# Optimization experiments

Measured on AMD Instinct MI355X. Metric: run time of the kernel, lower is better.

Reference implementation:

```python
import jax, jax.numpy as jnp
import numpy as np
import math

B, T, IN, H, OUT, L = 8, 256, 128, 128, 128, 2
MAX_EP_LEN = 10000.0


def _rotate(x, pos, d):
    # rope as in source: repeat(1,1,2) = concat along last dim (not interleave)
    half = jnp.exp(jnp.arange(0, d, 2, dtype=jnp.float32) * (-math.log(MAX_EP_LEN) / d))  # [d/2]
    ang = pos[..., None] * half  # [B,T,d/2]
    sine = jnp.concatenate([jnp.sin(ang), jnp.sin(ang)], axis=-1)
    cos = jnp.concatenate([jnp.cos(ang), jnp.cos(ang)], axis=-1)
    y1, y2 = jnp.split(x, 2, axis=-1)
    x_rot = jnp.concatenate([-y2, y1], axis=-1)
    return x * cos + x_rot * sine


def _layernorm(x, w, b, eps=1e-5):
    m = jnp.mean(x, axis=-1, keepdims=True)
    v = jnp.mean((x - m) ** 2, axis=-1, keepdims=True)
    return (x - m) / jnp.sqrt(v + eps) * w + b


def _block(x, S0, Z0, Wk, Wq, Wv, lw, lb, w1, b1, w2, b2, scw, scb):
    # x: [B,T,F]; S0: [B,F,F]; Z0: [B,F]
    x = _layernorm(x, lw, lb)
    K = jax.nn.elu(x @ Wk.T) + 1.0
    Q = jax.nn.elu(x @ Wq.T) + 1.0
    V = x @ Wv.T
    outer = jnp.einsum('bti,btj->btij', K, V)  # [B,T,F,F]
    S = jnp.clip(jnp.cumsum(outer, axis=1), -1e20, 1e20) + S0[:, None]  # [B,T,F,F]
    Z = jnp.clip(jnp.cumsum(K, axis=1), -1e20, 1e20) + Z0[:, None]      # [B,T,F]
    num = jnp.einsum('bti,btil->btl', Q, S)
    den = jnp.einsum('bti,bti->bt', Q, Z)[..., None] + 1e-5
    out = num / den
    out = jax.nn.relu(jax.nn.relu(out @ w1.T + b1) @ w2.T + b2)  # feed_forward
    out = out + x @ scw.T + scb                                   # residual shortcut
    return out, S[:, -1], Z[:, -1]


def setup_inputs() -> dict:
    key = jax.random.key(0)
    ks = jax.random.split(key, 14)
    s = 0.05
    return {
        'z': jax.random.normal(ks[0], (T, B, IN), jnp.float32),
        'state': jnp.zeros((B, L * (H * H + H) + 1), jnp.float32),
        'Wk': jax.random.normal(ks[1], (L, H, IN), jnp.float32) * s,
        'Wq': jax.random.normal(ks[2], (L, H, IN), jnp.float32) * s,
        'Wv': jax.random.normal(ks[3], (L, H, IN), jnp.float32) * s,
        'ln_w': jnp.ones((L, IN), jnp.float32),
        'ln_b': jnp.zeros((L, IN), jnp.float32),
        'ff_w1': jax.random.normal(ks[4], (L, H, H), jnp.float32) * s,
        'ff_b1': jnp.zeros((L, H), jnp.float32),
        'ff_w2': jax.random.normal(ks[5], (L, H, H), jnp.float32) * s,
        'ff_b2': jnp.zeros((L, H), jnp.float32),
        'sc_w': jax.random.normal(ks[6], (L, H, IN), jnp.float32) * s,
        'sc_b': jnp.zeros((L, H), jnp.float32),
        'unmap_w': jax.random.normal(ks[7], (OUT, H), jnp.float32) * s,
        'unmap_b': jnp.zeros((OUT,), jnp.float32),
    }


def reference(z, state, Wk, Wq, Wv, ln_w, ln_b, ff_w1, ff_b1, ff_w2, ff_b2, sc_w, sc_b, unmap_w, unmap_b):
    x = jnp.transpose(z, (1, 0, 2))  # [B,T,IN]
    ts = state[:, -1]                # [B] timestep counters
    core = state[:, :-1].reshape(B, L, H * H + H)
    pos = ts[:, None] + jnp.arange(T, dtype=jnp.float32)[None, :]  # [B,T]
    x = _rotate(x, pos, IN)  # embedding_type == 'rope'
    new_states = []
    for i in range(L):
        S0 = core[:, i, :H * H].reshape(B, H, H)
        Z0 = core[:, i, H * H:]
        x, Sl, Zl = _block(x, S0, Z0, Wk[i], Wq[i], Wv[i], ln_w[i], ln_b[i],
                           ff_w1[i], ff_b1[i], ff_w2[i], ff_b2[i], sc_w[i], sc_b[i])
        new_states.append(jnp.concatenate([Sl.reshape(B, -1), Zl], axis=-1))
    y = x @ unmap_w.T + unmap_b
    st = jnp.concatenate([jnp.stack(new_states, axis=1).reshape(B, -1), (ts + T)[:, None]], axis=-1)
    return jnp.transpose(y, (1, 0, 2)), st
```

## Files before the change

kernel.cpp:

```cpp
#include <hip/hip_runtime.h>
#include <math.h>

#define Bn 8
#define Tn 256
#define COREn 16512
#define SDn   33025

typedef __attribute__((ext_vector_type(8))) short short8;
typedef __attribute__((ext_vector_type(4))) short short4v;
typedef __attribute__((ext_vector_type(4))) float floatx4;

#define MFMA16(a,b,c) __builtin_amdgcn_mfma_f32_16x16x32_bf16(a,b,c,0,0,0)

static __device__ __forceinline__ unsigned short f2bf(float f) {
  unsigned int u = __float_as_uint(f);
  return (unsigned short)((u + 0x7FFFu + ((u >> 16) & 1u)) >> 16);
}
static __device__ __forceinline__ float bf2f(unsigned short h) {
  return __uint_as_float((unsigned int)h << 16);
}
static __device__ __forceinline__ short8 ldwfrag(const float* p) {
  float4 a = *(const float4*)p;
  float4 b = *(const float4*)(p + 4);
  short8 r;
  r[0] = (short)f2bf(a.x); r[1] = (short)f2bf(a.y);
  r[2] = (short)f2bf(a.z); r[3] = (short)f2bf(a.w);
  r[4] = (short)f2bf(b.x); r[5] = (short)f2bf(b.y);
  r[6] = (short)f2bf(b.z); r[7] = (short)f2bf(b.w);
  return r;
}
static __device__ __forceinline__ void ld8(const float* p, float* v) {
  float4 a = *(const float4*)p, b = *(const float4*)(p + 4);
  v[0]=a.x; v[1]=a.y; v[2]=a.z; v[3]=a.w; v[4]=b.x; v[5]=b.y; v[6]=b.z; v[7]=b.w;
}

static __device__ __forceinline__ void proj_epilogue(
    int by, int g0, int b, int t0l, int n0, int n1, int quad,
    floatx4 acc0, floatx4 acc1,
    unsigned short* __restrict__ Kb, unsigned short* __restrict__ Kt,
    unsigned short* __restrict__ Qb, unsigned short* __restrict__ Vt,
    unsigned short* __restrict__ skipb, const float* __restrict__ scb) {
  if (by == 0) {
    short4v kt0, kt1;
#pragma unroll
    for (int j = 0; j < 4; j++) {
      int row = quad * 4 + j;
      float e0 = acc0[j] > 0.f ? acc0[j] + 1.f : expf(acc0[j]);
      float e1 = acc1[j] > 0.f ? acc1[j] + 1.f : expf(acc1[j]);
      Kb[(size_t)(g0 + row) * 128 + n0] = f2bf(e0);
      Kb[(size_t)(g0 + row) * 128 + n1] = f2bf(e1);
      kt0[j] = (short)f2bf(e0); kt1[j] = (short)f2bf(e1);
    }
    *(short4v*)(Kt + (size_t)(b * 128 + n0) * 256 + t0l + quad * 4) = kt0;
    *(short4v*)(Kt + (size_t)(b * 128 + n1) * 256 + t0l + quad * 4) = kt1;
  } else if (by == 1) {
#pragma unroll
    for (int j = 0; j < 4; j++) {
      int row = quad * 4 + j;
      float e0 = acc0[j] > 0.f ? acc0[j] + 1.f : expf(acc0[j]);
      float e1 = acc1[j] > 0.f ? acc1[j] + 1.f : expf(acc1[j]);
      Qb[(size_t)(g0 + row) * 128 + n0] = f2bf(e0);
      Qb[(size_t)(g0 + row) * 128 + n1] = f2bf(e1);
    }
  } else if (by == 2) {
    short4v v0, v1;
#pragma unroll
    for (int j = 0; j < 4; j++) { v0[j] = (short)f2bf(acc0[j]); v1[j] = (short)f2bf(acc1[j]); }
    *(short4v*)(Vt + (size_t)(b * 128 + n0) * 256 + t0l + quad * 4) = v0;
    *(short4v*)(Vt + (size_t)(b * 128 + n1) * 256 + t0l + quad * 4) = v1;
  } else {
    float sb0 = scb[n0], sb1 = scb[n1];
#pragma unroll
    for (int j = 0; j < 4; j++) {
      int row = quad * 4 + j;
      skipb[(size_t)(g0 + row) * 128 + n0] = f2bf(acc0[j] + sb0);
      skipb[(size_t)(g0 + row) * 128 + n1] = f2bf(acc1[j] + sb1);
    }
  }
}

__global__ __launch_bounds__(256, 1) void prep_kernel(
    const float* __restrict__ z, const float* __restrict__ state,
    const float* __restrict__ Wk, const float* __restrict__ Wq,
    const float* __restrict__ Wv, const float* __restrict__ scw,
    const float* __restrict__ lnw, const float* __restrict__ lnb,
    const float* __restrict__ scb,
    const float* __restrict__ w1all, const float* __restrict__ w2all,
    const float* __restrict__ unw,
    unsigned short* __restrict__ Kb0, unsigned short* __restrict__ Qb0,
    unsigned short* __restrict__ Kt0, unsigned short* __restrict__ Vt0,
    unsigned short* __restrict__ skip0, unsigned short* __restrict__ S0t,
    float* __restrict__ warm_sink) {
  const int tid = threadIdx.x, bx = blockIdx.x;
  if (bx < 512) {
    __shared__ unsigned short xs[16][136];
    const int lane = tid & 63, wv = tid >> 6, lm = lane & 15, quad = lane >> 4;
    const int tile = bx >> 2, by = bx & 3;
    const int g0 = tile * 16;
    const int r = tid >> 4, c0 = (tid & 15) * 8;
    const int g = g0 + r, b = g >> 8, t = g & 255;
    const int n0 = wv * 32 + lm, n1 = n0 + 16;

    float v[8], pv[8];
    const float* zr = z + ((size_t)t * Bn + b) * 128;
    ld8(zr + c0, v);
    ld8(zr + (c0 ^ 64), pv);
    const float* W = by == 0 ? Wk : by == 1 ? Wq : by == 2 ? Wv : scw;
    short8 bA[4], bB[4];
#pragma unroll
    for (int kc = 0; kc < 4; kc++) {
      bA[kc] = ldwfrag(W + (size_t)n0 * 128 + kc * 32 + quad * 8);
      bB[kc] = ldwfrag(W + (size_t)n1 * 128 + kc * 32 + quad * 8);
    }
    float pos = state[(size_t)b * SDn + SDn - 1] + (float)t;

#pragma unroll
    for (int i = 0; i < 8; i++) {
      int jj = (c0 + i) & 63;
      float ang = pos * expf((float)jj * -0.14391156831212787f);
      float sn = sinf(ang), cs = cosf(ang);
      v[i] = (c0 < 64) ? (v[i] * cs - pv[i] * sn) : (v[i] * cs + pv[i] * sn);
    }
    float sm = 0.f, sq = 0.f;
#pragma unroll
    for (int i = 0; i < 8; i++) { sm += v[i]; sq += v[i] * v[i]; }
    for (int d = 8; d; d >>= 1) { sm += __shfl_xor(sm, d, 16); sq += __shfl_xor(sq, d, 16); }
    float mean = sm * (1.f / 128.f);
    float rstd = rsqrtf(sq * (1.f / 128.f) - mean * mean + 1e-5f);
    short8 xv;
#pragma unroll
    for (int i = 0; i < 8; i++)
      xv[i] = (short)f2bf((v[i] - mean) * rstd * lnw[c0 + i] + lnb[c0 + i]);
    *(short8*)&xs[r][c0] = xv;
    __syncthreads();

    const int bb = g0 >> 8, t0l = g0 & 255;
    floatx4 a0 = {0.f,0.f,0.f,0.f}, a1 = {0.f,0.f,0.f,0.f};
#pragma unroll
    for (int kc = 0; kc < 4; kc++) {
      short8 a = *(const short8*)&xs[lm][kc * 32 + quad * 8];
      a0 = MFMA16(a, bA[kc], a0);
      a1 = MFMA16(a, bB[kc], a1);
    }
    proj_epilogue(by, g0, bb, t0l, n0, n1, quad, a0, a1,
                  Kb0, Kt0, Qb0, Vt0, skip0, scb);
  } else if (bx < 528) {
    __shared__ float tl[32][33];
    const int id = bx - 512, b = id >> 1, l = id & 1;
    const float* src = state + (size_t)b * SDn + (size_t)l * COREn;
    unsigned short* dst = S0t + (size_t)(l * 8 + b) * 16384;
    const int r = tid >> 3, c4 = (tid & 7) * 4;
#pragma unroll
    for (int tI = 0; tI < 4; tI++)
      for (int tJ = 0; tJ < 4; tJ++) {
        int i0 = tI * 32, j0 = tJ * 32;
#pragma unroll
        for (int q = 0; q < 4; q++)
          tl[r][c4 + q] = src[(size_t)(i0 + r) * 128 + j0 + c4 + q];
        __syncthreads();
        short4v o;
#pragma unroll
        for (int q = 0; q < 4; q++) o[q] = (short)f2bf(tl[c4 + q][r]);
        *(short4v*)(dst + (size_t)(j0 + r) * 128 + i0 + c4) = o;
        __syncthreads();
      }
  } else {
    const int wb = bx - 528;
    const float* ptrs[9] = { w1all, w1all + 16384, w2all, w2all + 16384, unw,
                             Wk + 16384, Wq + 16384, Wv + 16384, scw + 16384 };
    float acc = 0.f;
#pragma unroll
    for (int i = 0; i < 9; i++) {
      float4 vv = ((const float4*)ptrs[i])[wb * 256 + tid];
      acc += vv.x + vv.y + vv.z + vv.w;
    }
    if (acc == 1234567.89f) warm_sink[0] = acc;
  }
}

static __device__ void state_upd(
    int tid, int idx, int l,
    const unsigned short* __restrict__ Kt, const unsigned short* __restrict__ Vt,
    const float* __restrict__ state, float* __restrict__ st_out) {
  const int lane = tid & 63, wv = tid >> 6, lm = lane & 15, quad = lane >> 4;
  const int b = idx >> 4, sub = idx & 15;
  const int i0 = (sub >> 1) * 16, j0 = (sub & 1) * 64;
  const size_t sb = (size_t)b * SDn + (size_t)l * COREn;
  short8 ka[8], vb[8];
#pragma unroll
  for (int kc = 0; kc < 8; kc++) {
    ka[kc] = *(const short8*)(Kt + (size_t)(b * 128 + i0 + lm) * 256 + kc * 32 + quad * 8);
    vb[kc] = *(const short8*)(Vt + (size_t)(b * 128 + j0 + wv * 16 + lm) * 256 + kc * 32 + quad * 8);
  }
  floatx4 acc = {0.f, 0.f, 0.f, 0.f};
#pragma unroll
  for (int kc = 0; kc < 8; kc++) acc = MFMA16(ka[kc], vb[kc], acc);
#pragma unroll
  for (int j = 0; j < 4; j++) {
    size_t off = sb + (size_t)(i0 + quad * 4 + j) * 128 + j0 + wv * 16 + lm;
    st_out[off] = acc[j] + state[off];
  }
  if (j0 == 0) {
    if (tid < 128) {
      int i = tid >> 3, seg = tid & 7;
      const unsigned short* kr = Kt + (size_t)(b * 128 + i0 + i) * 256 + seg * 32;
      float zs = 0.f;
#pragma unroll
      for (int x = 0; x < 4; x++) {
        short8 kv = *(const short8*)(kr + x * 8);
#pragma unroll
        for (int y = 0; y < 8; y++) zs += bf2f((unsigned short)kv[y]);
      }
      for (int d = 4; d; d >>= 1) zs += __shfl_xor(zs, d, 8);
      if (seg == 0) {
        size_t zo = sb + 16384 + i0 + i;
        st_out[zo] = zs + state[zo];
      }
    }
    if (sub == 0 && tid == 0 && l == 0)
      st_out[(size_t)b * SDn + SDn - 1] = state[(size_t)b * SDn + SDn - 1] + 256.f;
  }
}

__global__ __launch_bounds__(256, 1) void attn_kernel(
    const unsigned short* __restrict__ Kb, const unsigned short* __restrict__ Qb,
    const unsigned short* __restrict__ Vt, const unsigned short* __restrict__ Kt,
    const unsigned short* __restrict__ S0tl, const float* __restrict__ state,
    unsigned short* __restrict__ attnb, float* __restrict__ st_out, int l) {
  const int tid = threadIdx.x, bx = blockIdx.x;
  const int lane = tid & 63, wv = tid >> 6, lm = lane & 15, quad = lane >> 4;
  if (bx < 256) {
    __shared__ unsigned short xs[16][136];
    __shared__ unsigned short Ssc[4][16][40];
    __shared__ float Obuf[4][16][68];
    __shared__ float Z0s[128];
    __shared__ float denw[4][16];
    __shared__ float denz[16];
    __shared__ float dinv[16];

    const int tile = bx >> 1, half = bx & 1;
    const int b = tile >> 4, rt = tile & 15, t0 = rt * 16;
    const size_t sb = (size_t)b * SDn + (size_t)l * COREn;

    const int r = tid >> 4, cQ = (tid & 15) * 8;
    short8 qrow = *(const short8*)(Qb + (size_t)(b * 256 + t0 + r) * 128 + cQ);
    float z0v = (tid < 128) ? state[sb + 16384 + tid] : 0.f;

    const int nch = rt / 2 + 1;
    const bool hasA = (wv < nch), hasB = (wv + 4 < nch);
    const int kbA = (hasA ? wv : nch - 1) * 32;
    const int kbB = (hasB ? wv + 4 : nch - 1) * 32;
    short8 KA[8], KB[8], VA[4], VB[4], SF[4];
#pragma unroll
    for (int kc = 0; kc < 4; kc++) {
      KA[kc]     = *(const short8*)(Kb + (size_t)(b * 256 + kbA + lm) * 128 + kc * 32 + quad * 8);
      KA[4 + kc] = *(const short8*)(Kb + (size_t)(b * 256 + kbA + 16 + lm) * 128 + kc * 32 + quad * 8);
      KB[kc]     = *(const short8*)(Kb + (size_t)(b * 256 + kbB + lm) * 128 + kc * 32 + quad * 8);
      KB[4 + kc] = *(const short8*)(Kb + (size_t)(b * 256 + kbB + 16 + lm) * 128 + kc * 32 + quad * 8);
    }
#pragma unroll
    for (int jt = 0; jt < 4; jt++) {
      VA[jt] = *(const short8*)(Vt + (size_t)(b * 128 + half * 64 + jt * 16 + lm) * 256 + kbA + quad * 8);
      VB[jt] = *(const short8*)(Vt + (size_t)(b * 128 + half * 64 + jt * 16 + lm) * 256 + kbB + quad * 8);
      SF[jt] = *(const short8*)(S0tl + (size_t)b * 16384 +
                    (size_t)(half * 64 + jt * 16 + lm) * 128 + wv * 32 + quad * 8);
    }

    *(short8*)&xs[r][cQ] = qrow;
    if (tid < 128) Z0s[tid] = z0v;
    __syncthreads();

    { float qz = 0.f;
#pragma unroll
      for (int i = 0; i < 8; i++) qz += bf2f(xs[r][cQ + i]) * Z0s[cQ + i];
      for (int d = 8; d; d >>= 1) qz += __shfl_xor(qz, d, 16);
      if ((tid & 15) == 0) denz[r] = qz; }

    floatx4 oacc[4];
#pragma unroll
    for (int jt = 0; jt < 4; jt++) oacc[jt] = floatx4{0.f, 0.f, 0.f, 0.f};
    float dacc[4] = {0.f, 0.f, 0.f, 0.f};

    {
      floatx4 s0 = {0.f,0.f,0.f,0.f}, s1 = {0.f,0.f,0.f,0.f};
#pragma unroll
      for (int kc = 0; kc < 4; kc++) {
        short8 a = *(const short8*)&xs[lm][kc * 32 + quad * 8];
        s0 = MFMA16(a, KA[kc], s0);
        s1 = MFMA16(a, KA[4 + kc], s1);
      }
      const int tau0 = kbA + lm, tau1 = kbA + 16 + lm;
#pragma unroll
      for (int j = 0; j < 4; j++) {
        int m = t0 + quad * 4 + j;
        float v0 = (hasA && tau0 <= m) ? s0[j] : 0.f;
        float v1 = (hasA && tau1 <= m) ? s1[j] : 0.f;
        dacc[j] += v0 + v1;
        Ssc[wv][quad * 4 + j][lm]      = f2bf(v0);
        Ssc[wv][quad * 4 + j][16 + lm] = f2bf(v1);
      }
      short8 sa = *(const short8*)&Ssc[wv][lm][quad * 8];
#pragma unroll
      for (int jt = 0; jt < 4; jt++) oacc[jt] = MFMA16(sa, VA[jt], oacc[jt]);
    }
    {
      floatx4 s0 = {0.f,0.f,0.f,0.f}, s1 = {0.f,0.f,0.f,0.f};
#pragma unroll
      for (int kc = 0; kc < 4; kc++) {
        short8 a = *(const short8*)&xs[lm][kc * 32 + quad * 8];
        s0 = MFMA16(a, KB[kc], s0);
        s1 = MFMA16(a, KB[4 + kc], s1);
      }
      const int tau0 = kbB + lm, tau1 = kbB + 16 + lm;
#pragma unroll
      for (int j = 0; j < 4; j++) {
        int m = t0 + quad * 4 + j;
        float v0 = (hasB && tau0 <= m) ? s0[j] : 0.f;
        float v1 = (hasB && tau1 <= m) ? s1[j] : 0.f;
        dacc[j] += v0 + v1;
        Ssc[wv][quad * 4 + j][lm]      = f2bf(v0);
        Ssc[wv][quad * 4 + j][16 + lm] = f2bf(v1);
      }
      short8 sa = *(const short8*)&Ssc[wv][lm][quad * 8];
#pragma unroll
      for (int jt = 0; jt < 4; jt++) oacc[jt] = MFMA16(sa, VB[jt], oacc[jt]);
    }
    { short8 aq = *(const short8*)&xs[lm][wv * 32 + quad * 8];
#pragma unroll
      for (int jt = 0; jt < 4; jt++) oacc[jt] = MFMA16(aq, SF[jt], oacc[jt]); }

#pragma unroll
    for (int j = 0; j < 4; j++)
      for (int d = 8; d; d >>= 1) dacc[j] += __shfl_xor(dacc[j], d, 16);
    if (lm == 0) {
#pragma unroll
      for (int j = 0; j < 4; j++) denw[wv][quad * 4 + j] = dacc[j];
    }
#pragma unroll
    for (int jt = 0; jt < 4; jt++)
#pragma unroll
      for (int j = 0; j < 4; j++)
        Obuf[wv][quad * 4 + j][jt * 16 + lm] = oacc[jt][j];
    __syncthreads();
    if (tid < 16)
      dinv[tid] = 1.f / (denz[tid] + denw[0][tid] + denw[1][tid]
                         + denw[2][tid] + denw[3][tid] + 1e-5f);
    __syncthreads();
    { int rr = tid >> 4, c = (tid & 15) * 4;
      float di = dinv[rr];
      short4v ov;
#pragma unroll
      for (int q = 0; q < 4; q++) {
        float o = Obuf[0][rr][c + q] + Obuf[1][rr][c + q]
                + Obuf[2][rr][c + q] + Obuf[3][rr][c + q];
        ov[q] = (short)f2bf(o * di);
      }
      *(short4v*)(attnb + (size_t)(b * 256 + t0 + rr) * 128 + half * 64 + c) = ov; }
  } else {
    state_upd(tid, bx - 256, l, Kt, Vt, state, st_out);
  }
}

__global__ __launch_bounds__(256, 1) void ffproj_kernel(
    const unsigned short* __restrict__ attnb, const unsigned short* __restrict__ skipb,
    const float* __restrict__ w1, const float* __restrict__ b1,
    const float* __restrict__ w2, const float* __restrict__ b2,
    const float* __restrict__ lnw1, const float* __restrict__ lnb1,
    const float* __restrict__ Wk1, const float* __restrict__ Wq1,
    const float* __restrict__ Wv1, const float* __restrict__ scw1,
    const float* __restrict__ scb1,
    unsigned short* __restrict__ Kb1, unsigned short* __restrict__ Qb1,
    unsigned short* __restrict__ Kt1, unsigned short* __restrict__ Vt1,
    unsigned short* __restrict__ skip1) {
  __shared__ unsigned short xa[16][136];
  __shared__ unsigned short hs[16][136];
  __shared__ unsigned short xsl[16][136];
  __shared__ float os[16][132];
  const int tid = threadIdx.x, g0 = blockIdx.x * 16;
  const int lane = tid & 63, wv = tid >> 6, lm = lane & 15, quad = lane >> 4;
  const int n0 = wv * 32 + lm, n1 = n0 + 16;

  short8 w1A[4], w1B[4], w2A[4], w2B[4];
#pragma unroll
  for (int kc = 0; kc < 4; kc++) {
    w1A[kc] = ldwfrag(w1 + (size_t)n0 * 128 + kc * 32 + quad * 8);
    w1B[kc] = ldwfrag(w1 + (size_t)n1 * 128 + kc * 32 + quad * 8);
    w2A[kc] = ldwfrag(w2 + (size_t)n0 * 128 + kc * 32 + quad * 8);
    w2B[kc] = ldwfrag(w2 + (size_t)n1 * 128 + kc * 32 + quad * 8);
  }
  float bi10 = b1[n0], bi11 = b1[n1], bi20 = b2[n0], bi21 = b2[n1];
  float sk0[4], sk1[4];
#pragma unroll
  for (int j = 0; j < 4; j++) {
    sk0[j] = bf2f(skipb[(size_t)(g0 + quad * 4 + j) * 128 + n0]);
    sk1[j] = bf2f(skipb[(size_t)(g0 + quad * 4 + j) * 128 + n1]);
  }
  { int r = tid >> 4, c = (tid & 15) * 8;
    *(short8*)&xa[r][c] = *(const short8*)(attnb + (size_t)(g0 + r) * 128 + c); }
  __syncthreads();

  { floatx4 a0 = {0.f,0.f,0.f,0.f}, a1 = {0.f,0.f,0.f,0.f};
#pragma unroll
    for (int kc = 0; kc < 4; kc++) {
      short8 a = *(const short8*)&xa[lm][kc * 32 + quad * 8];
      a0 = MFMA16(a, w1A[kc], a0);
      a1 = MFMA16(a, w1B[kc], a1);
    }
#pragma unroll
    for (int j = 0; j < 4; j++) {
      int row = quad * 4 + j;
      hs[row][n0] = f2bf(fmaxf(a0[j] + bi10, 0.f));
      hs[row][n1] = f2bf(fmaxf(a1[j] + bi11, 0.f));
    } }
  __syncthreads();
  { floatx4 a0 = {0.f,0.f,0.f,0.f}, a1 = {0.f,0.f,0.f,0.f};
#pragma unroll
    for (int kc = 0; kc < 4; kc++) {
      short8 a = *(const short8*)&hs[lm][kc * 32 + quad * 8];
      a0 = MFMA16(a, w2A[kc], a0);
      a1 = MFMA16(a, w2B[kc], a1);
    }
#pragma unroll
    for (int j = 0; j < 4; j++) {
      int row = quad * 4 + j;
      os[row][n0] = fmaxf(a0[j] + bi20, 0.f) + sk0[j];
      os[row][n1] = fmaxf(a1[j] + bi21, 0.f) + sk1[j];
    } }
  __syncthreads();
  { int r = tid >> 4, c0 = (tid & 15) * 8;
    float v[8];
#pragma unroll
    for (int i = 0; i < 8; i++) v[i] = os[r][c0 + i];
    float sm = 0.f, sq = 0.f;
#pragma unroll
    for (int i = 0; i < 8; i++) { sm += v[i]; sq += v[i] * v[i]; }
    for (int d = 8; d; d >>= 1) { sm += __shfl_xor(sm, d, 16); sq += __shfl_xor(sq, d, 16); }
    float mean = sm * (1.f / 128.f);
    float rstd = rsqrtf(sq * (1.f / 128.f) - mean * mean + 1e-5f);
    short8 xv;
#pragma unroll
    for (int i = 0; i < 8; i++)
      xv[i] = (short)f2bf((v[i] - mean) * rstd * lnw1[c0 + i] + lnb1[c0 + i]);
    *(short8*)&xsl[r][c0] = xv; }
  __syncthreads();
  const int bb = g0 >> 8, t0l = g0 & 255;
#pragma unroll
  for (int by = 0; by < 4; by++) {
    const float* W = by == 0 ? Wk1 : by == 1 ? Wq1 : by == 2 ? Wv1 : scw1;
    short8 bA[4], bB[4];
#pragma unroll
    for (int kc = 0; kc < 4; kc++) {
      bA[kc] = ldwfrag(W + (size_t)n0 * 128 + kc * 32 + quad * 8);
      bB[kc] = ldwfrag(W + (size_t)n1 * 128 + kc * 32 + quad * 8);
    }
    floatx4 a0 = {0.f,0.f,0.f,0.f}, a1 = {0.f,0.f,0.f,0.f};
#pragma unroll
    for (int kc = 0; kc < 4; kc++) {
      short8 a = *(const short8*)&xsl[lm][kc * 32 + quad * 8];
      a0 = MFMA16(a, bA[kc], a0);
      a1 = MFMA16(a, bB[kc], a1);
    }
    proj_epilogue(by, g0, bb, t0l, n0, n1, quad, a0, a1,
                  Kb1, Kt1, Qb1, Vt1, skip1, scb1);
  }
}

__global__ __launch_bounds__(256, 1) void ffu_kernel(
    const unsigned short* __restrict__ attnb, const unsigned short* __restrict__ skipb,
    const float* __restrict__ w1, const float* __restrict__ b1,
    const float* __restrict__ w2, const float* __restrict__ b2,
    const float* __restrict__ unw, const float* __restrict__ unb,
    float* __restrict__ yout) {
  __shared__ unsigned short xa[16][136];
  __shared__ unsigned short hs[16][136];
  const int tid = threadIdx.x, g0 = blockIdx.x * 16;
  const int lane = tid & 63, wv = tid >> 6, lm = lane & 15, quad = lane >> 4;
  const int n0 = wv * 32 + lm, n1 = n0 + 16;

  short8 w1A[4], w1B[4], w2A[4], w2B[4], uA[4], uB[4];
#pragma unroll
  for (int kc = 0; kc < 4; kc++) {
    w1A[kc] = ldwfrag(w1 + (size_t)n0 * 128 + kc * 32 + quad * 8);
    w1B[kc] = ldwfrag(w1 + (size_t)n1 * 128 + kc * 32 + quad * 8);
    w2A[kc] = ldwfrag(w2 + (size_t)n0 * 128 + kc * 32 + quad * 8);
    w2B[kc] = ldwfrag(w2 + (size_t)n1 * 128 + kc * 32 + quad * 8);
    uA[kc]  = ldwfrag(unw + (size_t)n0 * 128 + kc * 32 + quad * 8);
    uB[kc]  = ldwfrag(unw + (size_t)n1 * 128 + kc * 32 + quad * 8);
  }
  float bi10 = b1[n0], bi11 = b1[n1], bi20 = b2[n0], bi21 = b2[n1];
  float u0b = unb[n0], u1b = unb[n1];
  float sk0[4], sk1[4];
#pragma unroll
  for (int j = 0; j < 4; j++) {
    sk0[j] = bf2f(skipb[(size_t)(g0 + quad * 4 + j) * 128 + n0]);
    sk1[j] = bf2f(skipb[(size_t)(g0 + quad * 4 + j) * 128 + n1]);
  }
  { int r = tid >> 4, c = (tid & 15) * 8;
    *(short8*)&xa[r][c] = *(const short8*)(attnb + (size_t)(g0 + r) * 128 + c); }
  __syncthreads();

  { floatx4 a0 = {0.f,0.f,0.f,0.f}, a1 = {0.f,0.f,0.f,0.f};
#pragma unroll
    for (int kc = 0; kc < 4; kc++) {
      short8 a = *(const short8*)&xa[lm][kc * 32 + quad * 8];
      a0 = MFMA16(a, w1A[kc], a0);
      a1 = MFMA16(a, w1B[kc], a1);
    }
#pragma unroll
    for (int j = 0; j < 4; j++) {
      int row = quad * 4 + j;
      hs[row][n0] = f2bf(fmaxf(a0[j] + bi10, 0.f));
      hs[row][n1] = f2bf(fmaxf(a1[j] + bi11, 0.f));
    } }
  __syncthreads();
  float o0[4], o1[4];
  { floatx4 a0 = {0.f,0.f,0.f,0.f}, a1 = {0.f,0.f,0.f,0.f};
#pragma unroll
    for (int kc = 0; kc < 4; kc++) {
      short8 a = *(const short8*)&hs[lm][kc * 32 + quad * 8];
      a0 = MFMA16(a, w2A[kc], a0);
      a1 = MFMA16(a, w2B[kc], a1);
    }
#pragma unroll
    for (int j = 0; j < 4; j++) {
      o0[j] = fmaxf(a0[j] + bi20, 0.f) + sk0[j];
      o1[j] = fmaxf(a1[j] + bi21, 0.f) + sk1[j];
    } }
  __syncthreads();
#pragma unroll
  for (int j = 0; j < 4; j++) {
    int row = quad * 4 + j;
    hs[row][n0] = f2bf(o0[j]);
    hs[row][n1] = f2bf(o1[j]);
  }
  __syncthreads();
  { floatx4 a0 = {0.f,0.f,0.f,0.f}, a1 = {0.f,0.f,0.f,0.f};
#pragma unroll
    for (int kc = 0; kc < 4; kc++) {
      short8 a = *(const short8*)&hs[lm][kc * 32 + quad * 8];
      a0 = MFMA16(a, uA[kc], a0);
      a1 = MFMA16(a, uB[kc], a1);
    }
#pragma unroll
    for (int j = 0; j < 4; j++) {
      int gg = g0 + quad * 4 + j;
      int bb = gg >> 8, tq = gg & 255;
      yout[(size_t)(tq * Bn + bb) * 128 + n0] = a0[j] + u0b;
      yout[(size_t)(tq * Bn + bb) * 128 + n1] = a1[j] + u1b;
    } }
}

extern "C" void kernel_launch(void* const* d_in, const int* in_sizes, int n_in,
                              void* d_out, int out_size, void* d_ws, size_t ws_size,
                              hipStream_t stream) {
  const float* z       = (const float*)d_in[0];
  const float* state   = (const float*)d_in[1];
  const float* Wk      = (const float*)d_in[2];
  const float* Wq      = (const float*)d_in[3];
  const float* Wv      = (const float*)d_in[4];
  const float* ln_w    = (const float*)d_in[5];
  const float* ln_b    = (const float*)d_in[6];
  const float* ff_w1   = (const float*)d_in[7];
  const float* ff_b1   = (const float*)d_in[8];
  const float* ff_w2   = (const float*)d_in[9];
  const float* ff_b2   = (const float*)d_in[10];
  const float* sc_w    = (const float*)d_in[11];
  const float* sc_b    = (const float*)d_in[12];
  const float* unmap_w = (const float*)d_in[13];
  const float* unmap_b = (const float*)d_in[14];

  float* y_out  = (float*)d_out;
  float* st_out = y_out + (size_t)Tn * Bn * 128;

  const size_t E = 262144;
  unsigned short* Kb0  = (unsigned short*)d_ws;
  unsigned short* Qb0  = Kb0 + E;
  unsigned short* Kt0  = Qb0 + E;
  unsigned short* Vt0  = Kt0 + E;
  unsigned short* Kb1  = Vt0 + E;
  unsigned short* Qb1  = Kb1 + E;
  unsigned short* Kt1  = Qb1 + E;
  unsigned short* Vt1  = Kt1 + E;
  unsigned short* skip0 = Vt1 + E;
  unsigned short* skip1 = skip0 + E;
  unsigned short* attnb = skip1 + E;
  unsigned short* S0t   = attnb + E;
  float* warm_sink = (float*)(S0t + (size_t)2 * 8 * 16384);

  prep_kernel<<<544, 256, 0, stream>>>(
      z, state, Wk, Wq, Wv, sc_w, ln_w, ln_b, sc_b,
      ff_w1, ff_w2, unmap_w,
      Kb0, Qb0, Kt0, Vt0, skip0, S0t, warm_sink);

  attn_kernel<<<384, 256, 0, stream>>>(
      Kb0, Qb0, Vt0, Kt0, S0t, state, attnb, st_out, 0);

  ffproj_kernel<<<128, 256, 0, stream>>>(
      attnb, skip0, ff_w1, ff_b1, ff_w2, ff_b2,
      ln_w + 128, ln_b + 128,
      Wk + 16384, Wq + 16384, Wv + 16384, sc_w + 16384, sc_b + 128,
      Kb1, Qb1, Kt1, Vt1, skip1);

  attn_kernel<<<384, 256, 0, stream>>>(
      Kb1, Qb1, Vt1, Kt1, S0t + (size_t)8 * 16384, state, attnb, st_out, 1);

  ffu_kernel<<<128, 256, 0, stream>>>(
      attnb, skip1, ff_w1 + 16384, ff_b1 + 128, ff_w2 + 16384, ff_b2 + 128,
      unmap_w, unmap_b, y_out);
}
```

Baseline: 133.8 us.

## Fuse all stages into one persistent kernel with atomic grid barriers

Replaces the five separate kernel launches with one persistent kernel of 256 blocks. A shared-memory union lets each stage reuse the same LDS, and stages are separated by atomic-counter grid barriers reset by a memset. The ffproj stage is split into an FF+layernorm unit writing xln1 and a separately distributed projection unit. The weight warm-up blocks are dropped. The aim is to remove launch gaps and tail idling, at the cost of spin-wait barriers, one block per CU, and reduced parallelism in some phases.

```diff
diff --git a/kernel.cpp b/kernel.cpp
--- a/kernel.cpp
+++ b/kernel.cpp
@@ -5,6 +5,7 @@
 #define Tn 256
 #define COREn 16512
 #define SDn   33025
+#define NBLK  256
 
 typedef __attribute__((ext_vector_type(8))) short short8;
 typedef __attribute__((ext_vector_type(4))) short short4v;
@@ -34,12 +35,37 @@
   v[0]=a.x; v[1]=a.y; v[2]=a.z; v[3]=a.w; v[4]=b.x; v[5]=b.y; v[6]=b.z; v[7]=b.w;
 }
 
+struct ProjS { unsigned short xs[16][136]; float tl[32][33]; };
+struct AttnS {
+  unsigned short xs[16][136];
+  unsigned short Ssc[4][16][40];
+  float Obuf[4][16][68];
+  float Z0s[128];
+  float denw[4][16];
+  float denz[16];
+  float dinv[16];
+};
+struct FfS { unsigned short xa[16][136]; unsigned short hs[16][136]; float os[16][132]; };
+union SmU { ProjS p; AttnS a; FfS f; };
+
+static __device__ __forceinline__ void gridbar(unsigned* cnt) {
+  __syncthreads();
+  if (threadIdx.x == 0) {
+    __threadfence();
+    __hip_atomic_fetch_add(cnt, 1u, __ATOMIC_ACQ_REL, __HIP_MEMORY_SCOPE_AGENT);
+    while (__hip_atomic_load(cnt, __ATOMIC_ACQUIRE, __HIP_MEMORY_SCOPE_AGENT) < (unsigned)NBLK)
+      __builtin_amdgcn_s_sleep(8);
+    __threadfence();
+  }
+  __syncthreads();
+}
+
 static __device__ __forceinline__ void proj_epilogue(
     int by, int g0, int b, int t0l, int n0, int n1, int quad,
     floatx4 acc0, floatx4 acc1,
-    unsigned short* __restrict__ Kb, unsigned short* __restrict__ Kt,
-    unsigned short* __restrict__ Qb, unsigned short* __restrict__ Vt,
-    unsigned short* __restrict__ skipb, const float* __restrict__ scb) {
+    unsigned short* Kb, unsigned short* Kt,
+    unsigned short* Qb, unsigned short* Vt,
+    unsigned short* skipb, const float* scb) {
   if (by == 0) {
     short4v kt0, kt1;
 #pragma unroll
@@ -79,109 +105,215 @@
   }
 }
 
-__global__ __launch_bounds__(256, 1) void prep_kernel(
-    const float* __restrict__ z, const float* __restrict__ state,
-    const float* __restrict__ Wk, const float* __restrict__ Wq,
-    const float* __restrict__ Wv, const float* __restrict__ scw,
-    const float* __restrict__ lnw, const float* __restrict__ lnb,
-    const float* __restrict__ scb,
-    const float* __restrict__ w1all, const float* __restrict__ w2all,
-    const float* __restrict__ unw,
-    unsigned short* __restrict__ Kb0, unsigned short* __restrict__ Qb0,
-    unsigned short* __restrict__ Kt0, unsigned short* __restrict__ Vt0,
-    unsigned short* __restrict__ skip0, unsigned short* __restrict__ S0t,
-    float* __restrict__ warm_sink) {
-  const int tid = threadIdx.x, bx = blockIdx.x;
-  if (bx < 512) {
-    __shared__ unsigned short xs[16][136];
-    const int lane = tid & 63, wv = tid >> 6, lm = lane & 15, quad = lane >> 4;
-    const int tile = bx >> 2, by = bx & 3;
-    const int g0 = tile * 16;
-    const int r = tid >> 4, c0 = (tid & 15) * 8;
-    const int g = g0 + r, b = g >> 8, t = g & 255;
-    const int n0 = wv * 32 + lm, n1 = n0 + 16;
-
-    float v[8], pv[8];
-    const float* zr = z + ((size_t)t * Bn + b) * 128;
-    ld8(zr + c0, v);
-    ld8(zr + (c0 ^ 64), pv);
-    const float* W = by == 0 ? Wk : by == 1 ? Wq : by == 2 ? Wv : scw;
-    short8 bA[4], bB[4];
+static __device__ void proj0_unit(
+    SmU& sm, int tid, int tile, int by,
+    const float* z, const float* state,
+    const float* Wk, const float* Wq, const float* Wv, const float* scw,
+    const float* lnw, const float* lnb, const float* scb,
+    unsigned short* Kb0, unsigned short* Qb0,
+    unsigned short* Kt0, unsigned short* Vt0, unsigned short* skip0) {
+  const int lane = tid & 63, wv = tid >> 6, lm = lane & 15, quad = lane >> 4;
+  const int g0 = tile * 16;
+  const int r = tid >> 4, c0 = (tid & 15) * 8;
+  const int g = g0 + r, b = g >> 8, t = g & 255;
+  const int n0 = wv * 32 + lm, n1 = n0 + 16;
+
+  float v[8], pv[8];
+  const float* zr = z + ((size_t)t * Bn + b) * 128;
+  ld8(zr + c0, v);
+  ld8(zr + (c0 ^ 64), pv);
+  const float* W = by == 0 ? Wk : by == 1 ? Wq : by == 2 ? Wv : scw;
+  short8 bA[4], bB[4];
+#pragma unroll
+  for (int kc = 0; kc < 4; kc++) {
+    bA[kc] = ldwfrag(W + (size_t)n0 * 128 + kc * 32 + quad * 8);
+    bB[kc] = ldwfrag(W + (size_t)n1 * 128 + kc * 32 + quad * 8);
+  }
+  float pos = state[(size_t)b * SDn + SDn - 1] + (float)t;
+#pragma unroll
+  for (int i = 0; i < 8; i++) {
+    int jj = (c0 + i) & 63;
+    float ang = pos * expf((float)jj * -0.14391156831212787f);
+    float sn = sinf(ang), cs = cosf(ang);
+    v[i] = (c0 < 64) ? (v[i] * cs - pv[i] * sn) : (v[i] * cs + pv[i] * sn);
+  }
+  float sm_ = 0.f, sq = 0.f;
+#pragma unroll
+  for (int i = 0; i < 8; i++) { sm_ += v[i]; sq += v[i] * v[i]; }
+  for (int d = 8; d; d >>= 1) { sm_ += __shfl_xor(sm_, d, 16); sq += __shfl_xor(sq, d, 16); }
+  float mean = sm_ * (1.f / 128.f);
+  float rstd = rsqrtf(sq * (1.f / 128.f) - mean * mean + 1e-5f);
+  short8 xv;
+#pragma unroll
+  for (int i = 0; i < 8; i++)
+    xv[i] = (short)f2bf((v[i] - mean) * rstd * lnw[c0 + i] + lnb[c0 + i]);
+  __syncthreads();
+  *(short8*)&sm.p.xs[r][c0] = xv;
+  __syncthreads();
+
+  const int bb = g0 >> 8, t0l = g0 & 255;
+  floatx4 a0 = {0.f,0.f,0.f,0.f}, a1 = {0.f,0.f,0.f,0.f};
+#pragma unroll
+  for (int kc = 0; kc < 4; kc++) {
+    short8 a = *(const short8*)&sm.p.xs[lm][kc * 32 + quad * 8];
+    a0 = MFMA16(a, bA[kc], a0);
+    a1 = MFMA16(a, bB[kc], a1);
+  }
+  proj_epilogue(by, g0, bb, t0l, n0, n1, quad, a0, a1,
+                Kb0, Kt0, Qb0, Vt0, skip0, scb);
+}
+
+static __device__ void s0t_unit(SmU& sm, int tid, int id,
+    const float* state, unsigned short* S0t) {
+  const int b = id >> 1, l = id & 1;
+  const float* src = state + (size_t)b * SDn + (size_t)l * COREn;
+  unsigned short* dst = S0t + (size_t)(l * 8 + b) * 16384;
+  const int r = tid >> 3, c4 = (tid & 7) * 4;
+  __syncthreads();
+#pragma unroll
+  for (int tI = 0; tI < 4; tI++)
+    for (int tJ = 0; tJ < 4; tJ++) {
+      int i0 = tI * 32, j0 = tJ * 32;
+#pragma unroll
+      for (int q = 0; q < 4; q++)
+        sm.p.tl[r][c4 + q] = src[(size_t)(i0 + r) * 128 + j0 + c4 + q];
+      __syncthreads();
+      short4v o;
+#pragma unroll
+      for (int q = 0; q < 4; q++) o[q] = (short)f2bf(sm.p.tl[c4 + q][r]);
+      *(short4v*)(dst + (size_t)(j0 + r) * 128 + i0 + c4) = o;
+      __syncthreads();
+    }
+}
+
+static __device__ void attn_unit(
+    SmU& sm, int tid, int unit, int l,
+    const unsigned short* Kb, const unsigned short* Qb,
+    const unsigned short* Vt, const unsigned short* S0tl,
+    const float* state, unsigned short* attnb) {
+  const int lane = tid & 63, wv = tid >> 6, lm = lane & 15, quad = lane >> 4;
+  const int tile = unit >> 1, half = unit & 1;
+  const int b = tile >> 4, rt = tile & 15, t0 = rt * 16;
+  const size_t sb = (size_t)b * SDn + (size_t)l * COREn;
+
+  const int r = tid >> 4, cQ = (tid & 15) * 8;
+  short8 qrow = *(const short8*)(Qb + (size_t)(b * 256 + t0 + r) * 128 + cQ);
+  float z0v = (tid < 128) ? state[sb + 16384 + tid] : 0.f;
+
+  const int nch = rt / 2 + 1;
+  const bool hasA = (wv < nch), hasB = (wv + 4 < nch);
+  const int kbA = (hasA ? wv : nch - 1) * 32;
+  const int kbB = (hasB ? wv + 4 : nch - 1) * 32;
+  short8 KA[8], KB[8], VA[4], VB[4], SF[4];
+#pragma unroll
+  for (int kc = 0; kc < 4; kc++) {
+    KA[kc]     = *(const short8*)(Kb + (size_t)(b * 256 + kbA + lm) * 128 + kc * 32 + quad * 8);
+    KA[4 + kc] = *(const short8*)(Kb + (size_t)(b * 256 + kbA + 16 + lm) * 128 + kc * 32 + quad * 8);
+    KB[kc]     = *(const short8*)(Kb + (size_t)(b * 256 + kbB + lm) * 128 + kc * 32 + quad * 8);
+    KB[4 + kc] = *(const short8*)(Kb + (size_t)(b * 256 + kbB + 16 + lm) * 128 + kc * 32 + quad * 8);
+  }
+#pragma unroll
+  for (int jt = 0; jt < 4; jt++) {
+    VA[jt] = *(const short8*)(Vt + (size_t)(b * 128 + half * 64 + jt * 16 + lm) * 256 + kbA + quad * 8);
+    VB[jt] = *(const short8*)(Vt + (size_t)(b * 128 + half * 64 + jt * 16 + lm) * 256 + kbB + quad * 8);
+    SF[jt] = *(const short8*)(S0tl + (size_t)b * 16384 +
+                  (size_t)(half * 64 + jt * 16 + lm) * 128 + wv * 32 + quad * 8);
+  }
+
+  *(short8*)&sm.a.xs[r][cQ] = qrow;
+  if (tid < 128) sm.a.Z0s[tid] = z0v;
+  __syncthreads();
+
+  { float qz = 0.f;
+#pragma unroll
+    for (int i = 0; i < 8; i++) qz += bf2f(sm.a.xs[r][cQ + i]) * sm.a.Z0s[cQ + i];
+    for (int d = 8; d; d >>= 1) qz += __shfl_xor(qz, d, 16);
+    if ((tid & 15) == 0) sm.a.denz[r] = qz; }
+
+  floatx4 oacc[4];
+#pragma unroll
+  for (int jt = 0; jt < 4; jt++) oacc[jt] = floatx4{0.f, 0.f, 0.f, 0.f};
+  float dacc[4] = {0.f, 0.f, 0.f, 0.f};
+
+  { floatx4 s0 = {0.f,0.f,0.f,0.f}, s1 = {0.f,0.f,0.f,0.f};
 #pragma unroll
     for (int kc = 0; kc < 4; kc++) {
-      bA[kc] = ldwfrag(W + (size_t)n0 * 128 + kc * 32 + quad * 8);
-      bB[kc] = ldwfrag(W + (size_t)n1 * 128 + kc * 32 + quad * 8);
-    }
-    float pos = state[(size_t)b * SDn + SDn - 1] + (float)t;
-
-#pragma unroll
-    for (int i = 0; i < 8; i++) {
-      int jj = (c0 + i) & 63;
-      float ang = pos * expf((float)jj * -0.14391156831212787f);
-      float sn = sinf(ang), cs = cosf(ang);
-      v[i] = (c0 < 64) ? (v[i] * cs - pv[i] * sn) : (v[i] * cs + pv[i] * sn);
-    }
-    float sm = 0.f, sq = 0.f;
-#pragma unroll
-    for (int i = 0; i < 8; i++) { sm += v[i]; sq += v[i] * v[i]; }
-    for (int d = 8; d; d >>= 1) { sm += __shfl_xor(sm, d, 16); sq += __shfl_xor(sq, d, 16); }
-    float mean = sm * (1.f / 128.f);
-    float rstd = rsqrtf(sq * (1.f / 128.f) - mean * mean + 1e-5f);
-    short8 xv;
-#pragma unroll
-    for (int i = 0; i < 8; i++)
-      xv[i] = (short)f2bf((v[i] - mean) * rstd * lnw[c0 + i] + lnb[c0 + i]);
-    *(short8*)&xs[r][c0] = xv;
-    __syncthreads();
-
-    const int bb = g0 >> 8, t0l = g0 & 255;
-    floatx4 a0 = {0.f,0.f,0.f,0.f}, a1 = {0.f,0.f,0.f,0.f};
+      short8 a = *(const short8*)&sm.a.xs[lm][kc * 32 + quad * 8];
+      s0 = MFMA16(a, KA[kc], s0);
+      s1 = MFMA16(a, KA[4 + kc], s1);
+    }
+    const int tau0 = kbA + lm, tau1 = kbA + 16 + lm;
+#pragma unroll
+    for (int j = 0; j < 4; j++) {
+      int m = t0 + quad * 4 + j;
+      float v0 = (hasA && tau0 <= m) ? s0[j] : 0.f;
+      float v1 = (hasA && tau1 <= m) ? s1[j] : 0.f;
+      dacc[j] += v0 + v1;
+      sm.a.Ssc[wv][quad * 4 + j][lm]      = f2bf(v0);
+      sm.a.Ssc[wv][quad * 4 + j][16 + lm] = f2bf(v1);
+    }
+    short8 sa = *(const short8*)&sm.a.Ssc[wv][lm][quad * 8];
+#pragma unroll
+    for (int jt = 0; jt < 4; jt++) oacc[jt] = MFMA16(sa, VA[jt], oacc[jt]);
+  }
+  { floatx4 s0 = {0.f,0.f,0.f,0.f}, s1 = {0.f,0.f,0.f,0.f};
 #pragma unroll
     for (int kc = 0; kc < 4; kc++) {
-      short8 a = *(const short8*)&xs[lm][kc * 32 + quad * 8];
-      a0 = MFMA16(a, bA[kc], a0);
-      a1 = MFMA16(a, bB[kc], a1);
-    }
-    proj_epilogue(by, g0, bb, t0l, n0, n1, quad, a0, a1,
-                  Kb0, Kt0, Qb0, Vt0, skip0, scb);
-  } else if (bx < 528) {
-    __shared__ float tl[32][33];
-    const int id = bx - 512, b = id >> 1, l = id & 1;
-    const float* src = state + (size_t)b * SDn + (size_t)l * COREn;
-    unsigned short* dst = S0t + (size_t)(l * 8 + b) * 16384;
-    const int r = tid >> 3, c4 = (tid & 7) * 4;
-#pragma unroll
-    for (int tI = 0; tI < 4; tI++)
-      for (int tJ = 0; tJ < 4; tJ++) {
-        int i0 = tI * 32, j0 = tJ * 32;
-#pragma unroll
-        for (int q = 0; q < 4; q++)
-          tl[r][c4 + q] = src[(size_t)(i0 + r) * 128 + j0 + c4 + q];
-        __syncthreads();
-        short4v o;
-#pragma unroll
-        for (int q = 0; q < 4; q++) o[q] = (short)f2bf(tl[c4 + q][r]);
-        *(short4v*)(dst + (size_t)(j0 + r) * 128 + i0 + c4) = o;
-        __syncthreads();
-      }
-  } else {
-    const int wb = bx - 528;
-    const float* ptrs[9] = { w1all, w1all + 16384, w2all, w2all + 16384, unw,
-                             Wk + 16384, Wq + 16384, Wv + 16384, scw + 16384 };
-    float acc = 0.f;
-#pragma unroll
-    for (int i = 0; i < 9; i++) {
-      float4 vv = ((const float4*)ptrs[i])[wb * 256 + tid];
-      acc += vv.x + vv.y + vv.z + vv.w;
-    }
-    if (acc == 1234567.89f) warm_sink[0] = acc;
-  }
-}
-
-static __device__ void state_upd(
+      short8 a = *(const short8*)&sm.a.xs[lm][kc * 32 + quad * 8];
+      s0 = MFMA16(a, KB[kc], s0);
+      s1 = MFMA16(a, KB[4 + kc], s1);
+    }
+    const int tau0 = kbB + lm, tau1 = kbB + 16 + lm;
+#pragma unroll
+    for (int j = 0; j < 4; j++) {
+      int m = t0 + quad * 4 + j;
+      float v0 = (hasB && tau0 <= m) ? s0[j] : 0.f;
+      float v1 = (hasB && tau1 <= m) ? s1[j] : 0.f;
+      dacc[j] += v0 + v1;
+      sm.a.Ssc[wv][quad * 4 + j][lm]      = f2bf(v0);
+      sm.a.Ssc[wv][quad * 4 + j][16 + lm] = f2bf(v1);
+    }
+    short8 sa = *(const short8*)&sm.a.Ssc[wv][lm][quad * 8];
+#pragma unroll
+    for (int jt = 0; jt < 4; jt++) oacc[jt] = MFMA16(sa, VB[jt], oacc[jt]);
+  }
+  { short8 aq = *(const short8*)&sm.a.xs[lm][wv * 32 + quad * 8];
+#pragma unroll
+    for (int jt = 0; jt < 4; jt++) oacc[jt] = MFMA16(aq, SF[jt], oacc[jt]); }
+
+#pragma unroll
+  for (int j = 0; j < 4; j++)
+    for (int d = 8; d; d >>= 1) dacc[j] += __shfl_xor(dacc[j], d, 16);
+  if (lm == 0) {
+#pragma unroll
+    for (int j = 0; j < 4; j++) sm.a.denw[wv][quad * 4 + j] = dacc[j];
+  }
+#pragma unroll
+  for (int jt = 0; jt < 4; jt++)
+#pragma unroll
+    for (int j = 0; j < 4; j++)
+      sm.a.Obuf[wv][quad * 4 + j][jt * 16 + lm] = oacc[jt][j];
+  __syncthreads();
+  if (tid < 16)
+    sm.a.dinv[tid] = 1.f / (sm.a.denz[tid] + sm.a.denw[0][tid] + sm.a.denw[1][tid]
+                            + sm.a.denw[2][tid] + sm.a.denw[3][tid] + 1e-5f);
+  __syncthreads();
+  { int rr = tid >> 4, c = (tid & 15) * 4;
+    float di = sm.a.dinv[rr];
+    short4v ov;
+#pragma unroll
+    for (int q = 0; q < 4; q++) {
+      float o = sm.a.Obuf[0][rr][c + q] + sm.a.Obuf[1][rr][c + q]
+              + sm.a.Obuf[2][rr][c + q] + sm.a.Obuf[3][rr][c + q];
+      ov[q] = (short)f2bf(o * di);
+    }
+    *(short4v*)(attnb + (size_t)(b * 256 + t0 + rr) * 128 + half * 64 + c) = ov; }
+}
+
+static __device__ void state_unit(
     int tid, int idx, int l,
-    const unsigned short* __restrict__ Kt, const unsigned short* __restrict__ Vt,
-    const float* __restrict__ state, float* __restrict__ st_out) {
+    const unsigned short* Kt, const unsigned short* Vt,
+    const float* state, float* st_out) {
   const int lane = tid & 63, wv = tid >> 6, lm = lane & 15, quad = lane >> 4;
   const int b = idx >> 4, sub = idx & 15;
   const int i0 = (sub >> 1) * 16, j0 = (sub & 1) * 64;
@@ -222,164 +354,13 @@
   }
 }
 
-__global__ __launch_bounds__(256, 1) void attn_kernel(
-    const unsigned short* __restrict__ Kb, const unsigned short* __restrict__ Qb,
-    const unsigned short* __restrict__ Vt, const unsigned short* __restrict__ Kt,
-    const unsigned short* __restrict__ S0tl, const float* __restrict__ state,
-    unsigned short* __restrict__ attnb, float* __restrict__ st_out, int l) {
-  const int tid = threadIdx.x, bx = blockIdx.x;
-  const int lane = tid & 63, wv = tid >> 6, lm = lane & 15, quad = lane >> 4;
-  if (bx < 256) {
-    __shared__ unsigned short xs[16][136];
-    __shared__ unsigned short Ssc[4][16][40];
-    __shared__ float Obuf[4][16][68];
-    __shared__ float Z0s[128];
-    __shared__ float denw[4][16];
-    __shared__ float denz[16];
-    __shared__ float dinv[16];
-
-    const int tile = bx >> 1, half = bx & 1;
-    const int b = tile >> 4, rt = tile & 15, t0 = rt * 16;
-    const size_t sb = (size_t)b * SDn + (size_t)l * COREn;
-
-    const int r = tid >> 4, cQ = (tid & 15) * 8;
-    short8 qrow = *(const short8*)(Qb + (size_t)(b * 256 + t0 + r) * 128 + cQ);
-    float z0v = (tid < 128) ? state[sb + 16384 + tid] : 0.f;
-
-    const int nch = rt / 2 + 1;
-    const bool hasA = (wv < nch), hasB = (wv + 4 < nch);
-    const int kbA = (hasA ? wv : nch - 1) * 32;
-    const int kbB = (hasB ? wv + 4 : nch - 1) * 32;
-    short8 KA[8], KB[8], VA[4], VB[4], SF[4];
-#pragma unroll
-    for (int kc = 0; kc < 4; kc++) {
-      KA[kc]     = *(const short8*)(Kb + (size_t)(b * 256 + kbA + lm) * 128 + kc * 32 + quad * 8);
-      KA[4 + kc] = *(const short8*)(Kb + (size_t)(b * 256 + kbA + 16 + lm) * 128 + kc * 32 + quad * 8);
-      KB[kc]     = *(const short8*)(Kb + (size_t)(b * 256 + kbB + lm) * 128 + kc * 32 + quad * 8);
-      KB[4 + kc] = *(const short8*)(Kb + (size_t)(b * 256 + kbB + 16 + lm) * 128 + kc * 32 + quad * 8);
-    }
-#pragma unroll
-    for (int jt = 0; jt < 4; jt++) {
-      VA[jt] = *(const short8*)(Vt + (size_t)(b * 128 + half * 64 + jt * 16 + lm) * 256 + kbA + quad * 8);
-      VB[jt] = *(const short8*)(Vt + (size_t)(b * 128 + half * 64 + jt * 16 + lm) * 256 + kbB + quad * 8);
-      SF[jt] = *(const short8*)(S0tl + (size_t)b * 16384 +
-                    (size_t)(half * 64 + jt * 16 + lm) * 128 + wv * 32 + quad * 8);
-    }
-
-    *(short8*)&xs[r][cQ] = qrow;
-    if (tid < 128) Z0s[tid] = z0v;
-    __syncthreads();
-
-    { float qz = 0.f;
-#pragma unroll
-      for (int i = 0; i < 8; i++) qz += bf2f(xs[r][cQ + i]) * Z0s[cQ + i];
-      for (int d = 8; d; d >>= 1) qz += __shfl_xor(qz, d, 16);
-      if ((tid & 15) == 0) denz[r] = qz; }
-
-    floatx4 oacc[4];
-#pragma unroll
-    for (int jt = 0; jt < 4; jt++) oacc[jt] = floatx4{0.f, 0.f, 0.f, 0.f};
-    float dacc[4] = {0.f, 0.f, 0.f, 0.f};
-
-    {
-      floatx4 s0 = {0.f,0.f,0.f,0.f}, s1 = {0.f,0.f,0.f,0.f};
-#pragma unroll
-      for (int kc = 0; kc < 4; kc++) {
-        short8 a = *(const short8*)&xs[lm][kc * 32 + quad * 8];
-        s0 = MFMA16(a, KA[kc], s0);
-        s1 = MFMA16(a, KA[4 + kc], s1);
-      }
-      const int tau0 = kbA + lm, tau1 = kbA + 16 + lm;
-#pragma unroll
-      for (int j = 0; j < 4; j++) {
-        int m = t0 + quad * 4 + j;
-        float v0 = (hasA && tau0 <= m) ? s0[j] : 0.f;
-        float v1 = (hasA && tau1 <= m) ? s1[j] : 0.f;
-        dacc[j] += v0 + v1;
-        Ssc[wv][quad * 4 + j][lm]      = f2bf(v0);
-        Ssc[wv][quad * 4 + j][16 + lm] = f2bf(v1);
-      }
-      short8 sa = *(const short8*)&Ssc[wv][lm][quad * 8];
-#pragma unroll
-      for (int jt = 0; jt < 4; jt++) oacc[jt] = MFMA16(sa, VA[jt], oacc[jt]);
-    }
-    {
-      floatx4 s0 = {0.f,0.f,0.f,0.f}, s1 = {0.f,0.f,0.f,0.f};
-#pragma unroll
-      for (int kc = 0; kc < 4; kc++) {
-        short8 a = *(const short8*)&xs[lm][kc * 32 + quad * 8];
-        s0 = MFMA16(a, KB[kc], s0);
-        s1 = MFMA16(a, KB[4 + kc], s1);
-      }
-      const int tau0 = kbB + lm, tau1 = kbB + 16 + lm;
-#pragma unroll
-      for (int j = 0; j < 4; j++) {
-        int m = t0 + quad * 4 + j;
-        float v0 = (hasB && tau0 <= m) ? s0[j] : 0.f;
-        float v1 = (hasB && tau1 <= m) ? s1[j] : 0.f;
-        dacc[j] += v0 + v1;
-        Ssc[wv][quad * 4 + j][lm]      = f2bf(v0);
-        Ssc[wv][quad * 4 + j][16 + lm] = f2bf(v1);
-      }
-      short8 sa = *(const short8*)&Ssc[wv][lm][quad * 8];
-#pragma unroll
-      for (int jt = 0; jt < 4; jt++) oacc[jt] = MFMA16(sa, VB[jt], oacc[jt]);
-    }
-    { short8 aq = *(const short8*)&xs[lm][wv * 32 + quad * 8];
-#pragma unroll
-      for (int jt = 0; jt < 4; jt++) oacc[jt] = MFMA16(aq, SF[jt], oacc[jt]); }
-
-#pragma unroll
-    for (int j = 0; j < 4; j++)
-      for (int d = 8; d; d >>= 1) dacc[j] += __shfl_xor(dacc[j], d, 16);
-    if (lm == 0) {
-#pragma unroll
-      for (int j = 0; j < 4; j++) denw[wv][quad * 4 + j] = dacc[j];
-    }
-#pragma unroll
-    for (int jt = 0; jt < 4; jt++)
-#pragma unroll
-      for (int j = 0; j < 4; j++)
-        Obuf[wv][quad * 4 + j][jt * 16 + lm] = oacc[jt][j];
-    __syncthreads();
-    if (tid < 16)
-      dinv[tid] = 1.f / (denz[tid] + denw[0][tid] + denw[1][tid]
-                         + denw[2][tid] + denw[3][tid] + 1e-5f);
-    __syncthreads();
-    { int rr = tid >> 4, c = (tid & 15) * 4;
-      float di = dinv[rr];
-      short4v ov;
-#pragma unroll
-      for (int q = 0; q < 4; q++) {
-        float o = Obuf[0][rr][c + q] + Obuf[1][rr][c + q]
-                + Obuf[2][rr][c + q] + Obuf[3][rr][c + q];
-        ov[q] = (short)f2bf(o * di);
-      }
-      *(short4v*)(attnb + (size_t)(b * 256 + t0 + rr) * 128 + half * 64 + c) = ov; }
-  } else {
-    state_upd(tid, bx - 256, l, Kt, Vt, state, st_out);
-  }
-}
-
-__global__ __launch_bounds__(256, 1) void ffproj_kernel(
-    const unsigned short* __restrict__ attnb, const unsigned short* __restrict__ skipb,
-    const float* __restrict__ w1, const float* __restrict__ b1,
-    const float* __restrict__ w2, const float* __restrict__ b2,
-    const float* __restrict__ lnw1, const float* __restrict__ lnb1,
-    const float* __restrict__ Wk1, const float* __restrict__ Wq1,
-    const float* __restrict__ Wv1, const float* __restrict__ scw1,
-    const float* __restrict__ scb1,
-    unsigned short* __restrict__ Kb1, unsigned short* __restrict__ Qb1,
-    unsigned short* __restrict__ Kt1, unsigned short* __restrict__ Vt1,
-    unsigned short* __restrict__ skip1) {
-  __shared__ unsigned short xa[16][136];
-  __shared__ unsigned short hs[16][136];
-  __shared__ unsigned short xsl[16][136];
-  __shared__ float os[16][132];
-  const int tid = threadIdx.x, g0 = blockIdx.x * 16;
+static __device__ void ffln_unit(
+    SmU& sm, int tid, int g0,
+    const unsigned short* attnb, const unsigned short* skipb,
+    const float* w1, const float* b1, const float* w2, const float* b2,
+    const float* lnw1, const float* lnb1, unsigned short* xln1) {
   const int lane = tid & 63, wv = tid >> 6, lm = lane & 15, quad = lane >> 4;
   const int n0 = wv * 32 + lm, n1 = n0 + 16;
-
   short8 w1A[4], w1B[4], w2A[4], w2B[4];
 #pragma unroll
   for (int kc = 0; kc < 4; kc++) {
@@ -396,87 +377,95 @@
     sk1[j] = bf2f(skipb[(size_t)(g0 + quad * 4 + j) * 128 + n1]);
   }
   { int r = tid >> 4, c = (tid & 15) * 8;
-    *(short8*)&xa[r][c] = *(const short8*)(attnb + (size_t)(g0 + r) * 128 + c); }
+    *(short8*)&sm.f.xa[r][c] = *(const short8*)(attnb + (size_t)(g0 + r) * 128 + c); }
   __syncthreads();
 
   { floatx4 a0 = {0.f,0.f,0.f,0.f}, a1 = {0.f,0.f,0.f,0.f};
 #pragma unroll
     for (int kc = 0; kc < 4; kc++) {
-      short8 a = *(const short8*)&xa[lm][kc * 32 + quad * 8];
+      short8 a = *(const short8*)&sm.f.xa[lm][kc * 32 + quad * 8];
       a0 = MFMA16(a, w1A[kc], a0);
       a1 = MFMA16(a, w1B[kc], a1);
     }
 #pragma unroll
     for (int j = 0; j < 4; j++) {
       int row = quad * 4 + j;
-      hs[row][n0] = f2bf(fmaxf(a0[j] + bi10, 0.f));
-      hs[row][n1] = f2bf(fmaxf(a1[j] + bi11, 0.f));
+      sm.f.hs[row][n0] = f2bf(fmaxf(a0[j] + bi10, 0.f));
+      sm.f.hs[row][n1] = f2bf(fmaxf(a1[j] + bi11, 0.f));
     } }
   __syncthreads();
   { floatx4 a0 = {0.f,0.f,0.f,0.f}, a1 = {0.f,0.f,0.f,0.f};
 #pragma unroll
     for (int kc = 0; kc < 4; kc++) {
-      short8 a = *(const short8*)&hs[lm][kc * 32 + quad * 8];
+      short8 a = *(const short8*)&sm.f.hs[lm][kc * 32 + quad * 8];
       a0 = MFMA16(a, w2A[kc], a0);
       a1 = MFMA16(a, w2B[kc], a1);
     }
 #pragma unroll
     for (int j = 0; j < 4; j++) {
       int row = quad * 4 + j;
-      os[row][n0] = fmaxf(a0[j] + bi20, 0.f) + sk0[j];
-      os[row][n1] = fmaxf(a1[j] + bi21, 0.f) + sk1[j];
+      sm.f.os[row][n0] = fmaxf(a0[j] + bi20, 0.f) + sk0[j];
+      sm.f.os[row][n1] = fmaxf(a1[j] + bi21, 0.f) + sk1[j];
     } }
   __syncthreads();
   { int r = tid >> 4, c0 = (tid & 15) * 8;
     float v[8];
 #pragma unroll
-    for (int i = 0; i < 8; i++) v[i] = os[r][c0 + i];
-    float sm = 0.f, sq = 0.f;
-#pragma unroll
-    for (int i = 0; i < 8; i++) { sm += v[i]; sq += v[i] * v[i]; }
-    for (int d = 8; d; d >>= 1) { sm += __shfl_xor(sm, d, 16); sq += __shfl_xor(sq, d, 16); }
-    float mean = sm * (1.f / 128.f);
+    for (int i = 0; i < 8; i++) v[i] = sm.f.os[r][c0 + i];
+    float sm_ = 0.f, sq = 0.f;
+#pragma unroll
+    for (int i = 0; i < 8; i++) { sm_ += v[i]; sq += v[i] * v[i]; }
+    for (int d = 8; d; d >>= 1) { sm_ += __shfl_xor(sm_, d, 16); sq += __shfl_xor(sq, d, 16); }
+    float mean = sm_ * (1.f / 128.f);
     float rstd = rsqrtf(sq * (1.f / 128.f) - mean * mean + 1e-5f);
     short8 xv;
 #pragma unroll
     for (int i = 0; i < 8; i++)
       xv[i] = (short)f2bf((v[i] - mean) * rstd * lnw1[c0 + i] + lnb1[c0 + i]);
-    *(short8*)&xsl[r][c0] = xv; }
+    *(short8*)(xln1 + (size_t)(g0 + r) * 128 + c0) = xv; }
+}
+
+static __device__ void proj1_unit(
+    SmU& sm, int tid, int tile, int by,
+    const unsigned short* xln1,
+    const float* Wk1, const float* Wq1, const float* Wv1, const float* scw1,
+    const float* scb1,
+    unsigned short* Kb1, unsigned short* Qb1,
+    unsigned short* Kt1, unsigned short* Vt1, unsigned short* skip1) {
+  const int lane = tid & 63, wv = tid >> 6, lm = lane & 15, quad = lane >> 4;
+  const int g0 = tile * 16;
+  const int n0 = wv * 32 + lm, n1 = n0 + 16;
+  const float* W = by == 0 ? Wk1 : by == 1 ? Wq1 : by == 2 ? Wv1 : scw1;
+  short8 bA[4], bB[4];
+#pragma unroll
+  for (int kc = 0; kc < 4; kc++) {
+    bA[kc] = ldwfrag(W + (size_t)n0 * 128 + kc * 32 + quad * 8);
+    bB[kc] = ldwfrag(W + (size_t)n1 * 128 + kc * 32 + quad * 8);
+  }
+  int r = tid >> 4, c = (tid & 15) * 8;
+  short8 xrow = *(const short8*)(xln1 + (size_t)(g0 + r) * 128 + c);
+  __syncthreads();
+  *(short8*)&sm.p.xs[r][c] = xrow;
   __syncthreads();
   const int bb = g0 >> 8, t0l = g0 & 255;
-#pragma unroll
-  for (int by = 0; by < 4; by++) {
-    const float* W = by == 0 ? Wk1 : by == 1 ? Wq1 : by == 2 ? Wv1 : scw1;
-    short8 bA[4], bB[4];
-#pragma unroll
-    for (int kc = 0; kc < 4; kc++) {
-      bA[kc] = ldwfrag(W + (size_t)n0 * 128 + kc * 32 + quad * 8);
-      bB[kc] = ldwfrag(W + (size_t)n1 * 128 + kc * 32 + quad * 8);
-    }
-    floatx4 a0 = {0.f,0.f,0.f,0.f}, a1 = {0.f,0.f,0.f,0.f};
-#pragma unroll
-    for (int kc = 0; kc < 4; kc++) {
-      short8 a = *(const short8*)&xsl[lm][kc * 32 + quad * 8];
-      a0 = MFMA16(a, bA[kc], a0);
-      a1 = MFMA16(a, bB[kc], a1);
-    }
-    proj_epilogue(by, g0, bb, t0l, n0, n1, quad, a0, a1,
-                  Kb1, Kt1, Qb1, Vt1, skip1, scb1);
-  }
-}
-
-__global__ __launch_bounds__(256, 1) void ffu_kernel(
-    const unsigned short* __restrict__ attnb, const unsigned short* __restrict__ skipb,
-    const float* __restrict__ w1, const float* __restrict__ b1,
-    const float* __restrict__ w2, const float* __restrict__ b2,
-    const float* __restrict__ unw, const float* __restrict__ unb,
-    float* __restrict__ yout) {
-  __shared__ unsigned short xa[16][136];
-  __shared__ unsigned short hs[16][136];
-  const int tid = threadIdx.x, g0 = blockIdx.x * 16;
+  floatx4 a0 = {0.f,0.f,0.f,0.f}, a1 = {0.f,0.f,0.f,0.f};
+#pragma unroll
+  for (int kc = 0; kc < 4; kc++) {
+    short8 a = *(const short8*)&sm.p.xs[lm][kc * 32 + quad * 8];
+    a0 = MFMA16(a, bA[kc], a0);
+    a1 = MFMA16(a, bB[kc], a1);
+  }
+  proj_epilogue(by, g0, bb, t0l, n0, n1, quad, a0, a1,
+                Kb1, Kt1, Qb1, Vt1, skip1, scb1);
+}
+
+static __device__ void ffu_unit(
+    SmU& sm, int tid, int g0,
+    const unsigned short* attnb, const unsigned short* skipb,
+    const float* w1, const float* b1, const float* w2, const float* b2,
+    const float* unw, const float* unb, float* yout) {
   const int lane = tid & 63, wv = tid >> 6, lm = lane & 15, quad = lane >> 4;
   const int n0 = wv * 32 + lm, n1 = n0 + 16;
-
   short8 w1A[4], w1B[4], w2A[4], w2B[4], uA[4], uB[4];
 #pragma unroll
   for (int kc = 0; kc < 4; kc++) {
@@ -496,28 +485,28 @@
     sk1[j] = bf2f(skipb[(size_t)(g0 + quad * 4 + j) * 128 + n1]);
   }
   { int r = tid >> 4, c = (tid & 15) * 8;
-    *(short8*)&xa[r][c] = *(const short8*)(attnb + (size_t)(g0 + r) * 128 + c); }
+    *(short8*)&sm.f.xa[r][c] = *(const short8*)(attnb + (size_t)(g0 + r) * 128 + c); }
   __syncthreads();
 
   { floatx4 a0 = {0.f,0.f,0.f,0.f}, a1 = {0.f,0.f,0.f,0.f};
 #pragma unroll
     for (int kc = 0; kc < 4; kc++) {
-      short8 a = *(const short8*)&xa[lm][kc * 32 + quad * 8];
+      short8 a = *(const short8*)&sm.f.xa[lm][kc * 32 + quad * 8];
       a0 = MFMA16(a, w1A[kc], a0);
       a1 = MFMA16(a, w1B[kc], a1);
     }
 #pragma unroll
     for (int j = 0; j < 4; j++) {
       int row = quad * 4 + j;
-      hs[row][n0] = f2bf(fmaxf(a0[j] + bi10, 0.f));
-      hs[row][n1] = f2bf(fmaxf(a1[j] + bi11, 0.f));
+      sm.f.hs[row][n0] = f2bf(fmaxf(a0[j] + bi10, 0.f));
+      sm.f.hs[row][n1] = f2bf(fmaxf(a1[j] + bi11, 0.f));
     } }
   __syncthreads();
   float o0[4], o1[4];
   { floatx4 a0 = {0.f,0.f,0.f,0.f}, a1 = {0.f,0.f,0.f,0.f};
 #pragma unroll
     for (int kc = 0; kc < 4; kc++) {
-      short8 a = *(const short8*)&hs[lm][kc * 32 + quad * 8];
+      short8 a = *(const short8*)&sm.f.hs[lm][kc * 32 + quad * 8];
       a0 = MFMA16(a, w2A[kc], a0);
       a1 = MFMA16(a, w2B[kc], a1);
     }
@@ -530,14 +519,14 @@
 #pragma unroll
   for (int j = 0; j < 4; j++) {
     int row = quad * 4 + j;
-    hs[row][n0] = f2bf(o0[j]);
-    hs[row][n1] = f2bf(o1[j]);
+    sm.f.hs[row][n0] = f2bf(o0[j]);
+    sm.f.hs[row][n1] = f2bf(o1[j]);
   }
   __syncthreads();
   { floatx4 a0 = {0.f,0.f,0.f,0.f}, a1 = {0.f,0.f,0.f,0.f};
 #pragma unroll
     for (int kc = 0; kc < 4; kc++) {
-      short8 a = *(const short8*)&hs[lm][kc * 32 + quad * 8];
+      short8 a = *(const short8*)&sm.f.hs[lm][kc * 32 + quad * 8];
       a0 = MFMA16(a, uA[kc], a0);
       a1 = MFMA16(a, uB[kc], a1);
     }
@@ -548,6 +537,58 @@
       yout[(size_t)(tq * Bn + bb) * 128 + n0] = a0[j] + u0b;
       yout[(size_t)(tq * Bn + bb) * 128 + n1] = a1[j] + u1b;
     } }
+}
+
+__global__ __launch_bounds__(256, 1) void persistent_kernel(
+    const float* z, const float* state,
+    const float* Wk, const float* Wq, const float* Wv,
+    const float* lnw, const float* lnb,
+    const float* w1, const float* b1, const float* w2, const float* b2,
+    const float* scw, const float* scb,
+    const float* unw, const float* unb,
+    float* yout, float* st_out,
+    unsigned short* Kb0, unsigned short* Qb0, unsigned short* Kt0, unsigned short* Vt0,
+    unsigned short* Kb1, unsigned short* Qb1, unsigned short* Kt1, unsigned short* Vt1,
+    unsigned short* skip0, unsigned short* skip1, unsigned short* attnb,
+    unsigned short* xln1, unsigned short* S0t, unsigned* bar) {
+  __shared__ SmU sm;
+  const int tid = threadIdx.x, bx = blockIdx.x;
+
+  { int u0 = 2 * bx, u1 = 2 * bx + 1;
+    proj0_unit(sm, tid, u0 >> 2, u0 & 3, z, state, Wk, Wq, Wv, scw,
+               lnw, lnb, scb, Kb0, Qb0, Kt0, Vt0, skip0);
+    proj0_unit(sm, tid, u1 >> 2, u1 & 3, z, state, Wk, Wq, Wv, scw,
+               lnw, lnb, scb, Kb0, Qb0, Kt0, Vt0, skip0);
+    if (bx < 16) s0t_unit(sm, tid, bx, state, S0t); }
+  gridbar(bar + 0);
+
+  attn_unit(sm, tid, bx, 0, Kb0, Qb0, Vt0, S0t, state, attnb);
+  gridbar(bar + 16);
+
+  if (bx < 128)
+    ffln_unit(sm, tid, bx * 16, attnb, skip0, w1, b1, w2, b2,
+              lnw + 128, lnb + 128, xln1);
+  else
+    state_unit(tid, bx - 128, 0, Kt0, Vt0, state, st_out);
+  gridbar(bar + 32);
+
+  { int u0 = 2 * bx, u1 = 2 * bx + 1;
+    proj1_unit(sm, tid, u0 >> 2, u0 & 3, xln1,
+               Wk + 16384, Wq + 16384, Wv + 16384, scw + 16384, scb + 128,
+               Kb1, Qb1, Kt1, Vt1, skip1);
+    proj1_unit(sm, tid, u1 >> 2, u1 & 3, xln1,
+               Wk + 16384, Wq + 16384, Wv + 16384, scw + 16384, scb + 128,
+               Kb1, Qb1, Kt1, Vt1, skip1); }
+  gridbar(bar + 48);
+
+  attn_unit(sm, tid, bx, 1, Kb1, Qb1, Vt1, S0t + (size_t)8 * 16384, state, attnb);
+  gridbar(bar + 64);
+
+  if (bx < 128)
+    ffu_unit(sm, tid, bx * 16, attnb, skip1,
+             w1 + 16384, b1 + 128, w2 + 16384, b2 + 128, unw, unb, yout);
+  else
+    state_unit(tid, bx - 128, 1, Kt1, Vt1, state, st_out);
 }
 
 extern "C" void kernel_launch(void* const* d_in, const int* in_sizes, int n_in,
@@ -573,38 +614,27 @@
   float* st_out = y_out + (size_t)Tn * Bn * 128;
 
   const size_t E = 262144;
-  unsigned short* Kb0  = (unsigned short*)d_ws;
-  unsigned short* Qb0  = Kb0 + E;
-  unsigned short* Kt0  = Qb0 + E;
-  unsigned short* Vt0  = Kt0 + E;
-  unsigned short* Kb1  = Vt0 + E;
-  unsigned short* Qb1  = Kb1 + E;
-  unsigned short* Kt1  = Qb1 + E;
-  unsigned short* Vt1  = Kt1 + E;
+  unsigned short* Kb0   = (unsigned short*)d_ws;
+  unsigned short* Qb0   = Kb0 + E;
+  unsigned short* Kt0   = Qb0 + E;
+  unsigned short* Vt0   = Kt0 + E;
+  unsigned short* Kb1   = Vt0 + E;
+  unsigned short* Qb1   = Kb1 + E;
+  unsigned short* Kt1   = Qb1 + E;
+  unsigned short* Vt1   = Kt1 + E;
   unsigned short* skip0 = Vt1 + E;
   unsigned short* skip1 = skip0 + E;
   unsigned short* attnb = skip1 + E;
-  unsigned short* S0t   = attnb + E;
-  float* warm_sink = (float*)(S0t + (size_t)2 * 8 * 16384);
-
-  prep_kernel<<<544, 256, 0, stream>>>(
-      z, state, Wk, Wq, Wv, sc_w, ln_w, ln_b, sc_b,
-      ff_w1, ff_w2, unmap_w,
-      Kb0, Qb0, Kt0, Vt0, skip0, S0t, warm_sink);
-
-  attn_kernel<<<384, 256, 0, stream>>>(
-      Kb0, Qb0, Vt0, Kt0, S0t, state, attnb, st_out, 0);
-
-  ffproj_kernel<<<128, 256, 0, stream>>>(
-      attnb, skip0, ff_w1, ff_b1, ff_w2, ff_b2,
-      ln_w + 128, ln_b + 128,
-      Wk + 16384, Wq + 16384, Wv + 16384, sc_w + 16384, sc_b + 128,
-      Kb1, Qb1, Kt1, Vt1, skip1);
-
-  attn_kernel<<<384, 256, 0, stream>>>(
-      Kb1, Qb1, Vt1, Kt1, S0t + (size_t)8 * 16384, state, attnb, st_out, 1);
-
-  ffu_kernel<<<128, 256, 0, stream>>>(
-      attnb, skip1, ff_w1 + 16384, ff_b1 + 128, ff_w2 + 16384, ff_b2 + 128,
-      unmap_w, unmap_b, y_out);
-}
+  unsigned short* xln1  = attnb + E;
+  unsigned short* S0t   = xln1 + E;
+  unsigned* bar = (unsigned*)(S0t + (size_t)2 * 8 * 16384);
+
+  hipMemsetAsync(bar, 0, 512, stream);
+
+  persistent_kernel<<<NBLK, 256, 0, stream>>>(
+      z, state, Wk, Wq, Wv, ln_w, ln_b,
+      ff_w1, ff_b1, ff_w2, ff_b2, sc_w, sc_b, unmap_w, unmap_b,
+      y_out, st_out,
+      Kb0, Qb0, Kt0, Vt0, Kb1, Qb1, Kt1, Vt1,
+      skip0, skip1, attnb, xln1, S0t, bar);
+}
```

Result: slower. 278.4 us (+108.0%).
